# Performance work log

Measured on AMD Instinct MI355X. Metric: run time of the kernel, lower is better.

Reference implementation:

```python
import jax, jax.numpy as jnp
import numpy as np


def ternarize(w):
    """TWN ternarization: delta=0.7*mean|w|, alpha = mean of |w| over kept entries."""
    aw = jnp.abs(w)
    delta = 0.7 * jnp.mean(aw)
    mask = (aw > delta).astype(w.dtype)
    alpha = jnp.sum(aw * mask) / jnp.maximum(jnp.sum(mask), 1.0)
    return alpha * jnp.sign(w) * mask


def conv3x3(x, w):
    # NCHW input, OIHW weight, stride 1, padding 1
    return jax.lax.conv_general_dilated(
        x, w, window_strides=(1, 1), padding=((1, 1), (1, 1)),
        dimension_numbers=("NCHW", "OIHW", "NCHW"))


def maxpool2(x):
    return jax.lax.reduce_window(
        x, -jnp.inf, jax.lax.max,
        window_dimensions=(1, 1, 2, 2), window_strides=(1, 1, 2, 2),
        padding="VALID")


def setup_inputs() -> dict:
    key = jax.random.key(0)
    ks = jax.random.split(key, 9)
    B = 4096
    return {
        "x":   jax.random.normal(ks[0], (B, 3, 32, 32), dtype=jnp.float32),
        "w1":  jax.random.normal(ks[1], (16, 3, 3, 3), dtype=jnp.float32) * 0.1,
        "b1":  jax.random.normal(ks[2], (16,), dtype=jnp.float32) * 0.01,
        "w2":  jax.random.normal(ks[3], (32, 16, 3, 3), dtype=jnp.float32) * 0.1,
        "b2":  jax.random.normal(ks[4], (32,), dtype=jnp.float32) * 0.01,
        "wf1": jax.random.normal(ks[5], (128, 32 * 8 * 8), dtype=jnp.float32) * 0.05,
        "bf1": jax.random.normal(ks[6], (128,), dtype=jnp.float32) * 0.01,
        "wf2": jax.random.normal(ks[7], (10, 128), dtype=jnp.float32) * 0.05,
        "bf2": jax.random.normal(ks[8], (10,), dtype=jnp.float32) * 0.01,
    }


def reference(x, w1, b1, w2, b2, wf1, bf1, wf2, bf2):
    h = jax.nn.relu(conv3x3(x, ternarize(w1)) + b1[None, :, None, None])
    h = maxpool2(h)                                    # [B,16,16,16]
    h = jax.nn.relu(conv3x3(h, ternarize(w2)) + b2[None, :, None, None])
    h = maxpool2(h)                                    # [B,32,8,8]
    h = h.reshape(-1, 32 * 8 * 8)
    h = jax.nn.relu(h @ ternarize(wf1).T + bf1)        # [B,128]
    return h @ ternarize(wf2).T + bf2                  # [B,10]
```

## Files before the change

### kernel.cpp

```cpp
#include <hip/hip_runtime.h>
#include <math.h>


typedef _Float16 half2v __attribute__((ext_vector_type(2)));
typedef _Float16 half4  __attribute__((ext_vector_type(4)));
typedef _Float16 half8  __attribute__((ext_vector_type(8)));
typedef float    f32x4  __attribute__((ext_vector_type(4)));
typedef unsigned u32x2  __attribute__((ext_vector_type(2)));

#define WF1_N 262144
#define WF1_SLICES 64
#define WF1_SLICE 4096

__device__ __forceinline__ float block_reduce_256(float v, float* red, int t) {
    red[t] = v; __syncthreads();
    for (int o = 128; o > 0; o >>= 1) {
        if (t < o) red[t] += red[t + o];
        __syncthreads();
    }
    float r = red[0]; __syncthreads();
    return r;
}

__device__ __forceinline__ float wave_sum64(float v) {
#pragma unroll
    for (int o = 32; o > 0; o >>= 1) v += __shfl_xor(v, o);
    return v;
}

__device__ __forceinline__ unsigned pk16(float a, float b) {
    half2v h;
    h[0] = (_Float16)a;
    h[1] = (_Float16)b;
    return __builtin_bit_cast(unsigned, h);
}

__global__ void tern_stageA(const float* __restrict__ w1,
                            const float* __restrict__ w2,
                            const float* __restrict__ wf1,
                            const float* __restrict__ wf2,
                            _Float16* __restrict__ tw1f,
                            _Float16* __restrict__ tw2f,
                            float* __restrict__ twf2,
                            float* __restrict__ part_sum) {
    __shared__ float red[256];
    const int t = threadIdx.x;
    const int bid = blockIdx.x;

    if (bid < WF1_SLICES) {
        const float4* src = reinterpret_cast<const float4*>(wf1 + (size_t)bid * WF1_SLICE);
        float s = 0.f;
#pragma unroll
        for (int j = 0; j < 4; ++j) {
            const float4 v = src[t + j * 256];
            s += fabsf(v.x) + fabsf(v.y) + fabsf(v.z) + fabsf(v.w);
        }
        const float tot = block_reduce_256(s, red, t);
        if (t == 0) part_sum[bid] = tot;
        return;
    }

    const float* w;
    int n;
    const int which = bid - WF1_SLICES;
    switch (which) {
        case 0: w = w1;  n = 432;  break;
        case 1: w = w2;  n = 4608; break;
        default: w = wf2; n = 1280; break;
    }
    float s = 0.f;
    for (int i = t; i < n; i += 256) s += fabsf(w[i]);
    const float delta = 0.7f * block_reduce_256(s, red, t) / (float)n;
    float sa = 0.f, cnt = 0.f;
    for (int i = t; i < n; i += 256) {
        float a = fabsf(w[i]);
        if (a > delta) { sa += a; cnt += 1.f; }
    }
    const float tot_sa = block_reduce_256(sa, red, t);
    const float tot_cnt = block_reduce_256(cnt, red, t);
    const float alpha = tot_sa / fmaxf(tot_cnt, 1.0f);

    switch (which) {
        case 0:
            for (int o = t; o < 768; o += 256) {
                int j = o & 3;
                int l = (o >> 2) & 63;
                int m = o >> 8;
                int rho = m * 4 + (l >> 4);
                int co = l & 15;
                float v = 0.f;
                if (rho < 9 && j < 3) {
                    float wv = w1[co * 27 + (rho / 3) * 9 + (rho % 3) * 3 + j];
                    v = (fabsf(wv) > delta) ? copysignf(alpha, wv) : 0.f;
                }
                tw1f[o] = (_Float16)v;
            }
            break;
        case 1:
            for (int o = t; o < 4608; o += 256) {
                int j  = o & 3;
                int ll = (o >> 2) & 63;
                int nt = (o >> 8) & 1;
                int s9 = o >> 9;
                int ci = (ll >> 4) * 4 + j;
                int co = (ll & 15) + nt * 16;
                float wv = w2[(co * 16 + ci) * 9 + s9];
                float v = (fabsf(wv) > delta) ? copysignf(alpha, wv) : 0.f;
                tw2f[o] = (_Float16)v;
            }
            break;
        default:
            for (int o = t; o < 1280; o += 256) {
                float wv = wf2[o];
                twf2[o] = (fabsf(wv) > delta) ? copysignf(alpha, wv) : 0.f;
            }
            break;
    }
}

__global__ void tern_stageB(const float* __restrict__ wf1,
                            const float* __restrict__ part_sum,
                            float* __restrict__ part_sa,
                            float* __restrict__ part_cnt,
                            _Float16* __restrict__ twf1) {
    __shared__ float red[256];
    const int t = threadIdx.x;
    const int bid = blockIdx.x;

    float v = (t < WF1_SLICES) ? part_sum[t] : 0.f;
    const float delta = 0.7f * block_reduce_256(v, red, t) / (float)WF1_N;

    const float4* src = reinterpret_cast<const float4*>(wf1 + (size_t)bid * WF1_SLICE);
    half4* dst = reinterpret_cast<half4*>(twf1 + (size_t)bid * WF1_SLICE);
    float sa = 0.f, cnt = 0.f;
#pragma unroll
    for (int j = 0; j < 4; ++j) {
        const float4 w4 = src[t + j * 256];
        half4 hv;
        float a;
        a = fabsf(w4.x); if (a > delta) { sa += a; cnt += 1.f; }
        hv[0] = (_Float16)((fabsf(w4.x) > delta) ? copysignf(1.0f, w4.x) : 0.f);
        a = fabsf(w4.y); if (a > delta) { sa += a; cnt += 1.f; }
        hv[1] = (_Float16)((fabsf(w4.y) > delta) ? copysignf(1.0f, w4.y) : 0.f);
        a = fabsf(w4.z); if (a > delta) { sa += a; cnt += 1.f; }
        hv[2] = (_Float16)((fabsf(w4.z) > delta) ? copysignf(1.0f, w4.z) : 0.f);
        a = fabsf(w4.w); if (a > delta) { sa += a; cnt += 1.f; }
        hv[3] = (_Float16)((fabsf(w4.w) > delta) ? copysignf(1.0f, w4.w) : 0.f);
        dst[t + j * 256] = hv;
    }
    const float tot_sa = block_reduce_256(sa, red, t);
    const float tot_cnt = block_reduce_256(cnt, red, t);
    if (t == 0) { part_sa[bid] = tot_sa; part_cnt[bid] = tot_cnt; }
}

#define H1P 18
#define PSZ 3472
#define H1SZ (18*18*H1P)

__global__ __launch_bounds__(256, 5)
void conv12_kernel(const float* __restrict__ x,
                   const float* __restrict__ b1,
                   const float* __restrict__ b2,
                   const _Float16* __restrict__ tw1f,
                   const _Float16* __restrict__ tw2f,
                   _Float16* __restrict__ h2p) {
    __shared__ __align__(16) _Float16 PA[PSZ];
    __shared__ __align__(16) _Float16 PB[PSZ];
    __shared__ __align__(16) _Float16 h1s[H1SZ];
    __shared__ __align__(16) _Float16 h2s[2048];
    __shared__ float b1s[16], b2s[32];

    const int t = threadIdx.x;
    const int b = blockIdx.x;
    const int wid = t >> 6, l = t & 63;

    float4 xv4[3];
    {
        const float4* xb4 = reinterpret_cast<const float4*>(x + (size_t)b * 3072);
#pragma unroll
        for (int j = 0; j < 3; ++j) xv4[j] = xb4[t + j * 256];
    }
    half4 bfr1[3];
#pragma unroll
    for (int m = 0; m < 3; ++m)
        bfr1[m] = *reinterpret_cast<const half4*>(tw1f + (size_t)(m * 64 + l) * 4);
    if (t < 16) b1s[t] = b1[t];
    if (t < 32) b2s[t] = b2[t];

    {
        const float4 z = {0.f, 0.f, 0.f, 0.f};
        float4* pa4 = reinterpret_cast<float4*>(PA);
        float4* pb4 = reinterpret_cast<float4*>(PB);
        float4* h14 = reinterpret_cast<float4*>(h1s);
        for (int i = t; i < PSZ * 2 / 16; i += 256) { pa4[i] = z; pb4[i] = z; }
        for (int i = t; i < H1SZ * 2 / 16; i += 256) h14[i] = z;
    }
    __syncthreads();

    {
#pragma unroll
        for (int j = 0; j < 3; ++j) {
            const int f = t + j * 256;
            const int c = f >> 8, rem = f & 255;
            const int iy = rem >> 3, ix = (rem & 7) << 2;
            const int idx = ((c * 34) + iy + 1) * 34 + 1 + ix;
            const float4 v = xv4[j];
            const unsigned w0 = __builtin_bit_cast(unsigned, __builtin_amdgcn_cvt_pkrtz(v.x, v.y));
            const unsigned w1 = __builtin_bit_cast(unsigned, __builtin_amdgcn_cvt_pkrtz(v.z, v.w));
            const half2v h0 = __builtin_bit_cast(half2v, w0);
            const half2v h1 = __builtin_bit_cast(half2v, w1);
            *reinterpret_cast<unsigned*>(&PB[idx - 1]) = w0;
            *reinterpret_cast<unsigned*>(&PB[idx + 1]) = w1;
            PA[idx] = h0[0];
            *reinterpret_cast<unsigned*>(&PA[idx + 1]) = (w0 >> 16) | (w1 << 16);
            PA[idx + 3] = h1[1];
        }
    }
    __syncthreads();

    {
        const int r15 = l & 15, g = l >> 4;
        const int p = r15 & 1;
        int laneIdx[3];
#pragma unroll
        for (int m = 0; m < 3; ++m) {
            int rho = m * 4 + g;
            if (rho > 8) rho = 0;
            const int c = rho / 3, ky = rho % 3;
            laneIdx[m] = ((c * 34 + ky) * 34 + r15 - p) >> 1;
        }
        const unsigned* basep = p ? reinterpret_cast<const unsigned*>(PB)
                                  : reinterpret_cast<const unsigned*>(PA);
        const float bia = b1s[r15];

#pragma unroll 1
        for (int i = 0; i < 8; ++i) {
            const int P = wid * 8 + i;
            const int py = P >> 1, xh = P & 1;
            const int x0 = xh * 16;
            f32x4 accA = {0.f, 0.f, 0.f, 0.f};
            f32x4 accB = {0.f, 0.f, 0.f, 0.f};
#pragma unroll
            for (int h2 = 0; h2 < 2; ++h2) {
                const int y = 2 * py + h2;
                const int uoff = (y * 34 + x0) >> 1;
                f32x4 acc = {0.f, 0.f, 0.f, 0.f};
#pragma unroll
                for (int m = 0; m < 3; ++m) {
                    const unsigned* q = basep + laneIdx[m] + uoff;
                    u32x2 d;
                    d.x = q[0];
                    d.y = q[1];
                    const half4 a = __builtin_bit_cast(half4, d);
                    acc = __builtin_amdgcn_mfma_f32_16x16x16f16(a, bfr1[m], acc, 0, 0, 0);
                }
                if (h2 == 0) accA = acc; else accB = acc;
            }
            float e0 = fmaxf(fmaxf(accA[0], accA[1]), fmaxf(accB[0], accB[1]));
            float e1 = fmaxf(fmaxf(accA[2], accA[3]), fmaxf(accB[2], accB[3]));
            e0 = fmaxf(e0 + bia, 0.f);
            e1 = fmaxf(e1 + bia, 0.f);
            const int px0 = xh * 8 + g * 2;
            const int pix = (py + 1) * 18 + (px0 + 1);
            h1s[pix * H1P + r15]       = (_Float16)e0;
            h1s[(pix + 1) * H1P + r15] = (_Float16)e1;
        }
    }

    half4 bfr[9][2];
#pragma unroll
    for (int s = 0; s < 9; ++s)
#pragma unroll
        for (int nt = 0; nt < 2; ++nt)
            bfr[s][nt] = *reinterpret_cast<const half4*>(
                tw2f + (size_t)((s * 2 + nt) * 64 + l) * 4);
    __syncthreads();

    {
        const int xq = l & 15, g = l >> 4;
        const unsigned* h1u = reinterpret_cast<const unsigned*>(h1s);
        float sav[2][2];
#pragma unroll
        for (int yy = 0; yy < 4; ++yy) {
            const int y = wid * 4 + yy;
            const unsigned* qb = h1u + (y * 18 + xq) * 9 + g * 2;
            f32x4 acc0 = {0.f, 0.f, 0.f, 0.f};
            f32x4 acc1 = {0.f, 0.f, 0.f, 0.f};
#pragma unroll
            for (int s = 0; s < 9; ++s) {
                const int dy = s / 3, dx = s % 3;
                const int off = (dy * 18 + dx) * 9;
                u32x2 d;
                d.x = qb[off];
                d.y = qb[off + 1];
                const half4 a = __builtin_bit_cast(half4, d);
                acc0 = __builtin_amdgcn_mfma_f32_16x16x16f16(a, bfr[s][0], acc0, 0, 0, 0);
                acc1 = __builtin_amdgcn_mfma_f32_16x16x16f16(a, bfr[s][1], acc1, 0, 0, 0);
            }
            const float p00 = fmaxf(acc0[0], acc0[1]);
            const float p01 = fmaxf(acc0[2], acc0[3]);
            const float p10 = fmaxf(acc1[0], acc1[1]);
            const float p11 = fmaxf(acc1[2], acc1[3]);
            if ((yy & 1) == 0) {
                sav[0][0] = p00; sav[0][1] = p01;
                sav[1][0] = p10; sav[1][1] = p11;
            } else {
                const int py = (wid * 4 + yy) >> 1;
                const float v00 = fmaxf(fmaxf(sav[0][0], p00) + b2s[xq], 0.f);
                const float v01 = fmaxf(fmaxf(sav[0][1], p01) + b2s[xq], 0.f);
                const float v10 = fmaxf(fmaxf(sav[1][0], p10) + b2s[xq + 16], 0.f);
                const float v11 = fmaxf(fmaxf(sav[1][1], p11) + b2s[xq + 16], 0.f);
                unsigned* h2u = reinterpret_cast<unsigned*>(h2s);
                h2u[xq * 32 + py * 4 + g]        = pk16(v00, v01);
                h2u[(xq + 16) * 32 + py * 4 + g] = pk16(v10, v11);
            }
        }
    }
    __syncthreads();

    {
        const float4 v = reinterpret_cast<const float4*>(h2s)[t];
        reinterpret_cast<float4*>(h2p + (size_t)b * 2048)[t] = v;
    }
}

__global__ __launch_bounds__(1024, 4)
void fc_kernel(const _Float16* __restrict__ h2p,
               const _Float16* __restrict__ twf1,
               const float* __restrict__ part_sa,
               const float* __restrict__ part_cnt,
               const float* __restrict__ bf1,
               const float* __restrict__ twf2,
               const float* __restrict__ bf2,
               float* __restrict__ out) {
    __shared__ float red[8][2048];

    const int t = threadIdx.x;
    const int wid = t >> 6, l = t & 63;
    const int lx = l & 15, g = l >> 4;
    const int m0 = blockIdx.x * 16;

    float alphaW = 0.f;
    if (wid == 0) {
        const float tsa = wave_sum64(part_sa[l]);
        const float tcn = wave_sum64(part_cnt[l]);
        alphaW = tsa / fmaxf(tcn, 1.0f);
    }

    f32x4 acc[8];
#pragma unroll
    for (int nt = 0; nt < 8; ++nt) acc[nt] = (f32x4){0.f, 0.f, 0.f, 0.f};

    const int kb = wid * 128;
#pragma unroll
    for (int it = 0; it < 4; ++it) {
        const int k0 = kb + it * 32;
        const half8 a = *reinterpret_cast<const half8*>(
            h2p + (size_t)(m0 + lx) * 2048 + k0 + g * 8);
#pragma unroll
        for (int nt = 0; nt < 8; ++nt) {
            const half8 bb = *reinterpret_cast<const half8*>(
                twf1 + (size_t)(nt * 16 + lx) * 2048 + k0 + g * 8);
            acc[nt] = __builtin_amdgcn_mfma_f32_16x16x32_f16(a, bb, acc[nt], 0, 0, 0);
        }
    }

    for (int h = 8; h >= 1; h >>= 1) {
        if (wid >= h && wid < 2 * h) {
            float* dst = &red[wid - h][0];
#pragma unroll
            for (int nt = 0; nt < 8; ++nt)
                *reinterpret_cast<f32x4*>(dst + nt * 256 + l * 4) = acc[nt];
        }
        __syncthreads();
        if (wid < h) {
            const float* srcp = &red[wid][0];
#pragma unroll
            for (int nt = 0; nt < 8; ++nt) {
                const f32x4 v = *reinterpret_cast<const f32x4*>(srcp + nt * 256 + l * 4);
                acc[nt] += v;
            }
        }
        __syncthreads();
    }

    if (wid == 0) {
#pragma unroll
        for (int nt = 0; nt < 8; ++nt) {
            const int col = nt * 16 + lx;
            const float bias = bf1[col];
#pragma unroll
            for (int r = 0; r < 4; ++r)
                red[0][(g * 4 + r) * 128 + col] = fmaxf(acc[nt][r] * alphaW + bias, 0.f);
        }
    }
    __syncthreads();

    if (t < 160) {
        const int m = t / 10, n = t % 10;
        float a = bf2[n];
#pragma unroll 8
        for (int k = 0; k < 128; ++k) a += red[0][m * 128 + k] * twf2[n * 128 + k];
        out[(size_t)(m0 + m) * 10 + n] = a;
    }
}

extern "C" void kernel_launch(void* const* d_in, const int* in_sizes, int n_in,
                              void* d_out, int out_size, void* d_ws, size_t ws_size,
                              hipStream_t stream) {
    const float* x   = (const float*)d_in[0];
    const float* w1  = (const float*)d_in[1];
    const float* b1  = (const float*)d_in[2];
    const float* w2  = (const float*)d_in[3];
    const float* b2  = (const float*)d_in[4];
    const float* wf1 = (const float*)d_in[5];
    const float* bf1 = (const float*)d_in[6];
    const float* wf2 = (const float*)d_in[7];
    const float* bf2 = (const float*)d_in[8];
    float* out = (float*)d_out;
    const int B = in_sizes[0] / (3 * 32 * 32);

    char* ws = (char*)d_ws;
    _Float16*  tw1f  = (_Float16*)(ws + 0);
    _Float16*  tw2f  = (_Float16*)(ws + 1536);
    _Float16*  twf1  = (_Float16*)(ws + 10752);
    float*     twf2  = (float*)(ws + 535040);
    _Float16*  h2p   = (_Float16*)(ws + 540160);
    float*     part_sum = (float*)(ws + 17317376);
    float*     part_sa  = part_sum + 64;
    float*     part_cnt = part_sa + 64;

    tern_stageA<<<WF1_SLICES + 3, 256, 0, stream>>>(w1, w2, wf1, wf2,
                                                    tw1f, tw2f, twf2, part_sum);
    tern_stageB<<<WF1_SLICES, 256, 0, stream>>>(wf1, part_sum, part_sa, part_cnt, twf1);
    conv12_kernel<<<B, 256, 0, stream>>>(x, b1, b2, tw1f, tw2f, h2p);
    fc_kernel<<<B / 16, 1024, 0, stream>>>(h2p, twf1, part_sa, part_cnt,
                                           bf1, twf2, bf2, out);
}
```

Baseline: 71.23 us.

## Restructure FC kernel: stage activations in LDS, split N across waves, shrink reduction

The FC1 work split changes. Previously each wave owned a 128-wide K slice and all 128 output columns, followed by a four-level tree reduction through 64KB of LDS. Now waves are split 4 ways over K and 4 ways over N (32 columns each), the 16-row activation tile is staged into padded LDS in two halves, and only a single-level reduction of 3 partials is needed. This lowers accumulator register pressure, the number of reduction barriers and LDS reduction traffic. In exchange it adds staging barriers and drops the occupancy hint from 4 to 2.

```diff
diff --git a/kernel.cpp b/kernel.cpp
--- a/kernel.cpp
+++ b/kernel.cpp
@@ -324,7 +324,9 @@
     }
 }
 
-__global__ __launch_bounds__(1024, 4)
+#define FC_PAD 8
+
+__global__ __launch_bounds__(1024, 2)
 void fc_kernel(const _Float16* __restrict__ h2p,
                const _Float16* __restrict__ twf1,
                const float* __restrict__ part_sa,
@@ -333,65 +335,66 @@
                const float* __restrict__ twf2,
                const float* __restrict__ bf2,
                float* __restrict__ out) {
-    __shared__ float red[8][2048];
+    __shared__ __align__(16) _Float16 As[16][1024 + FC_PAD];
+    __shared__ float red[4][3][2][256];
+    __shared__ float Hs[16][132];
 
     const int t = threadIdx.x;
     const int wid = t >> 6, l = t & 63;
+    const int kq = wid & 3, ng = wid >> 2;
     const int lx = l & 15, g = l >> 4;
     const int m0 = blockIdx.x * 16;
 
-    float alphaW = 0.f;
-    if (wid == 0) {
-        const float tsa = wave_sum64(part_sa[l]);
-        const float tcn = wave_sum64(part_cnt[l]);
-        alphaW = tsa / fmaxf(tcn, 1.0f);
-    }
-
-    f32x4 acc[8];
-#pragma unroll
-    for (int nt = 0; nt < 8; ++nt) acc[nt] = (f32x4){0.f, 0.f, 0.f, 0.f};
-
-    const int kb = wid * 128;
-#pragma unroll
-    for (int it = 0; it < 4; ++it) {
-        const int k0 = kb + it * 32;
-        const half8 a = *reinterpret_cast<const half8*>(
-            h2p + (size_t)(m0 + lx) * 2048 + k0 + g * 8);
-#pragma unroll
-        for (int nt = 0; nt < 8; ++nt) {
-            const half8 bb = *reinterpret_cast<const half8*>(
-                twf1 + (size_t)(nt * 16 + lx) * 2048 + k0 + g * 8);
-            acc[nt] = __builtin_amdgcn_mfma_f32_16x16x32_f16(a, bb, acc[nt], 0, 0, 0);
-        }
-    }
-
-    for (int h = 8; h >= 1; h >>= 1) {
-        if (wid >= h && wid < 2 * h) {
-            float* dst = &red[wid - h][0];
-#pragma unroll
-            for (int nt = 0; nt < 8; ++nt)
-                *reinterpret_cast<f32x4*>(dst + nt * 256 + l * 4) = acc[nt];
+    const float alphaW = wave_sum64(part_sa[l]) / fmaxf(wave_sum64(part_cnt[l]), 1.0f);
+
+    f32x4 acc[2];
+    acc[0] = (f32x4){0.f, 0.f, 0.f, 0.f};
+    acc[1] = (f32x4){0.f, 0.f, 0.f, 0.f};
+
+    const int stg_r = t >> 7;
+    const int stg_c = (t & 127) * 8;
+
+#pragma unroll
+    for (int h = 0; h < 2; ++h) {
+        if (h) __syncthreads();
+#pragma unroll
+        for (int p = 0; p < 2; ++p) {
+            const int r = stg_r + p * 8;
+            *reinterpret_cast<float4*>(&As[r][stg_c]) =
+                *reinterpret_cast<const float4*>(
+                    h2p + (size_t)(m0 + r) * 2048 + h * 1024 + stg_c);
         }
         __syncthreads();
-        if (wid < h) {
-            const float* srcp = &red[wid][0];
-#pragma unroll
-            for (int nt = 0; nt < 8; ++nt) {
-                const f32x4 v = *reinterpret_cast<const f32x4*>(srcp + nt * 256 + l * 4);
-                acc[nt] += v;
-            }
-        }
-        __syncthreads();
-    }
-
-    if (wid == 0) {
-#pragma unroll
-        for (int nt = 0; nt < 8; ++nt) {
-            const int col = nt * 16 + lx;
+#pragma unroll
+        for (int it = 0; it < 8; ++it) {
+            const int kk = kq * 256 + it * 32;
+            const half8 a = *reinterpret_cast<const half8*>(&As[lx][kk + g * 8]);
+#pragma unroll
+            for (int nt = 0; nt < 2; ++nt) {
+                const half8 bb = *reinterpret_cast<const half8*>(
+                    twf1 + (size_t)(ng * 32 + nt * 16 + lx) * 2048 + h * 1024 + kk + g * 8);
+                acc[nt] = __builtin_amdgcn_mfma_f32_16x16x32_f16(a, bb, acc[nt], 0, 0, 0);
+            }
+        }
+    }
+
+    if (kq != 0) {
+#pragma unroll
+        for (int nt = 0; nt < 2; ++nt)
+            *reinterpret_cast<f32x4*>(&red[ng][kq - 1][nt][l * 4]) = acc[nt];
+    }
+    __syncthreads();
+    if (kq == 0) {
+#pragma unroll
+        for (int nt = 0; nt < 2; ++nt) {
+#pragma unroll
+            for (int q = 0; q < 3; ++q)
+                acc[nt] += *reinterpret_cast<const f32x4*>(&red[ng][q][nt][l * 4]);
+            const int col = ng * 32 + nt * 16 + lx;
             const float bias = bf1[col];
 #pragma unroll
             for (int r = 0; r < 4; ++r)
-                red[0][(g * 4 + r) * 128 + col] = fmaxf(acc[nt][r] * alphaW + bias, 0.f);
+                Hs[g * 4 + r][col] = fmaxf(acc[nt][r] * alphaW + bias, 0.f);
         }
     }
     __syncthreads();
@@ -400,7 +403,7 @@
         const int m = t / 10, n = t % 10;
         float a = bf2[n];
 #pragma unroll 8
-        for (int k = 0; k < 128; ++k) a += red[0][m * 128 + k] * twf2[n * 128 + k];
+        for (int k = 0; k < 128; ++k) a += Hs[m][k] * twf2[n * 128 + k];
         out[(size_t)(m0 + m) * 10 + n] = a;
     }
 }
```

Measured after the change: 72.35 us. No clear change (+1.6%).
